# Kernel tuning notes

Hardware: AMD Instinct MI355X
Metric: run time of the kernel (lower is better)

## Reference

```python
import jax, jax.numpy as jnp
import numpy as np
from jax import lax

GEN_POLY = ("1111001", "1011011")  # rate 1/2, constraint length 7 (octal 171/133)


def build_trellis(gen_poly):
    """Feed-forward (non-recursive) convolutional trellis tables.

    State = shift-register contents, most-recent bit is the MSB of the state
    index. Returns int32 tables, each [ns, ni]:
      to_nodes[s, b]        : next state from state s with input bit b
      op_by_fromnode[s, b]  : emitted output-symbol index for (s, b)
      from_nodes[j, m]      : m-th predecessor state of state j
      ip_by_tonode[j, m]    : input bit taken on that predecessor transition
    """
    mu = len(gen_poly[0]) - 1
    ns, ni = 2 ** mu, 2
    g = np.array([[int(c) for c in p] for p in gen_poly])  # [conv_n, mu+1]
    to_nodes = np.zeros((ns, ni), np.int32)
    op_by_fromnode = np.zeros((ns, ni), np.int32)
    from_nodes = np.zeros((ns, ni), np.int32)
    ip_by_tonode = np.zeros((ns, ni), np.int32)
    fill = np.zeros(ns, np.int32)
    for s in range(ns):
        rbits = [(s >> (mu - 1 - j)) & 1 for j in range(mu)]
        for b in range(ni):
            w = np.array([b] + rbits)                 # full window [b, r0..r_{mu-1}]
            obits = (g @ w) % 2                        # output bits, MSB first
            o = int("".join(str(int(x)) for x in obits), 2)
            j = int("".join(str(x) for x in ([b] + rbits[:-1])), 2)
            to_nodes[s, b] = j
            op_by_fromnode[s, b] = o
            from_nodes[j, fill[j]] = s
            ip_by_tonode[j, fill[j]] = b
            fill[j] += 1
    return to_nodes, op_by_fromnode, from_nodes, ip_by_tonode


TO_NODES, OP_BY_FROM, FROM_NODES, IP_BY_TO = build_trellis(GEN_POLY)
CONV_N = len(GEN_POLY)
MU = len(GEN_POLY[0]) - 1
NS = 2 ** MU
NO = 2 ** CONV_N
# output-symbol bit patterns, MSB first, mapped to signs (1-2*bit)
_OP_BITS = np.array([[(o >> (CONV_N - 1 - j)) & 1 for j in range(CONV_N)]
                     for o in range(NO)], np.float32)
OP_SIGN = jnp.asarray(1.0 - 2.0 * _OP_BITS)  # [NO, CONV_N]
IP_SIGN = jnp.asarray([1.0, -1.0])           # sign of input bit b: 1-2b


def setup_inputs() -> dict:
    key = jax.random.key(0)
    k1, k2 = jax.random.split(key)
    B, n = 256, 4096
    T = n // CONV_N  # = k = 2048 info bits
    llr_ch = jax.random.normal(k1, (B, n), dtype=jnp.float32)
    llr_a = jax.random.normal(k2, (B, T), dtype=jnp.float32)
    return {"llr_ch": llr_ch, "llr_a": llr_a}


def _bcjr(llr_ch, llr_a):
    B, n = llr_ch.shape
    T = n // CONV_N
    # branch metrics: bm[t, b, o] = exp(0.5 * sum_j llr[b, t, j] * (1-2*opbit_j(o)))
    llr_r = llr_ch.reshape(B, T, CONV_N)
    bm = jnp.exp(0.5 * jnp.einsum('btj,oj->tbo', llr_r, OP_SIGN))  # [T, B, NO]
    llr_a_t = llr_a.T  # [T, B]

    def gamma_fn(bm_t, la_t):
        # a-priori factor exp(0.5*llr_a*(1-2b)) times channel branch metric
        ap = jnp.exp(0.5 * la_t[:, None, None] * IP_SIGN[None, None, :])  # [B,1,2]
        return ap * bm_t[:, OP_BY_FROM]  # [B, NS, 2]

    alpha0 = jnp.zeros((B, NS), jnp.float32).at[:, 0].set(1.0)

    def fwd(alpha_prev, inp):
        bm_t, la_t = inp
        gam = gamma_fn(bm_t, la_t)                        # [B, NS, 2] by from-state
        ag = gam * alpha_prev[:, :, None]                  # alpha_{t} * gamma_t
        agt = ag[:, FROM_NODES, IP_BY_TO]                  # regroup by to-state
        alpha = agt.sum(-1)
        alpha = alpha / alpha.sum(-1, keepdims=True)       # normalize (as in TF code)
        return alpha, alpha_prev                            # emit alpha BEFORE step t

    _, alphas = lax.scan(fwd, alpha0, (bm, llr_a_t))       # alphas[t] = alpha_t, [T,B,NS]

    beta_T = jnp.full((B, NS), 1.0 / NS, jnp.float32)      # non-terminated: uniform

    def bwd(beta_next, inp):
        bm_t, la_t, alpha_t = inp
        gam = gamma_fn(bm_t, la_t)                         # [B, NS, 2]
        bg = gam * beta_next[:, TO_NODES]                  # gamma * beta_{t+1}(to)
        beta = bg.sum(-1)
        beta = beta / beta.sum(-1, keepdims=True)
        joint = alpha_t[:, :, None] * bg                   # APP per (state, bit)
        llr_t = jnp.log(joint[..., 0].sum(-1)) - jnp.log(joint[..., 1].sum(-1))
        return beta, llr_t

    _, llrs_rev = lax.scan(bwd, beta_T, (bm[::-1], llr_a_t[::-1], alphas[::-1]))
    return llrs_rev[::-1].T  # [B, T] soft LLRs (hard_out=False)


def reference(llr_ch, llr_a):
    return _bcjr(llr_ch, llr_a)
```

## Files before the change

### kernel.cpp

```cpp
#include <hip/hip_runtime.h>
#include <hip/hip_bf16.h>

#define T_LEN 2048
#define NSTATE 64
#define NCHUNK 16
#define CH_S 128
#define WARM 64
#define RK 16

__device__ __forceinline__ float wave_sum64(float v) {
    #pragma unroll
    for (int d = 1; d < 64; d <<= 1) v += __shfl_xor(v, d, 64);
    return v;
}

__device__ __forceinline__ float pair_sum_xor1(float v) {
    int r = __builtin_amdgcn_update_dpp(0, __float_as_int(v), 0xB1, 0xF, 0xF, true);
    return v + __int_as_float(r);
}

__device__ __forceinline__ unsigned short bf16_of(float f) {
    return (unsigned short)((__float_as_uint(f) + 0x8000u) >> 16);
}
__device__ __forceinline__ float bf16_lo(unsigned u) { return __uint_as_float(u << 16); }
__device__ __forceinline__ float bf16_hi(unsigned u) { return __uint_as_float(u & 0xffff0000u); }


__global__ __launch_bounds__(256, 8)
void bcjr_sweep_kernel(const float* __restrict__ llr_ch,
                       const float* __restrict__ llr_a,
                       unsigned short* __restrict__ wsA,
                       unsigned short* __restrict__ wsB)
{
    const int wave  = blockIdx.x * 4 + (threadIdx.x >> 6);
    const int lane  = threadIdx.x & 63;
    const int dir   = wave & 1;
    const int chunk = (wave >> 1) & (NCHUNK - 1);
    const int b     = wave >> 5;

    const float c0 = 1.0f - 2.0f * (float)(__popc(lane & 57) & 1);
    const float c1 = 1.0f - 2.0f * (float)(__popc(lane & 27) & 1);
    const float kE = 0.5f * 1.442695040888963f;
    const float k0 = kE * c0, k1 = kE * c1;

    const float* chp = llr_ch + (size_t)b * (2 * T_LEN);
    const float* lap = llr_a  + (size_t)b * T_LEN;

    if (dir == 0) {
        unsigned short* w = wsA + (size_t)b * T_LEN * NSTATE;
        const int  fs0 = 2 * (lane & 31);
        const bool fhi = (lane >= 32);
        const int t0 = chunk * CH_S;
        const int ts = (chunk == 0) ? t0 : t0 - WARM;
        float state = (chunk == 0) ? ((lane == 0) ? 1.0f : 0.0f) : (1.0f / 64.0f);

        for (int g = ts; g < t0 + CH_S; g += RK) {
            const bool store = (g >= t0);
            #pragma unroll
            for (int h = 0; h < 2; ++h) {
                const int gb = g + 8 * h;
                const float4* c4 = (const float4*)(chp + 2 * gb);
                const float4* a4 = (const float4*)(lap + gb);
                float4 cc[4], aa[2];
                #pragma unroll
                for (int i = 0; i < 4; ++i) cc[i] = c4[i];
                #pragma unroll
                for (int i = 0; i < 2; ++i) aa[i] = a4[i];
                unsigned short* wb = w + (size_t)gb * NSTATE + lane;
                #pragma unroll
                for (int i = 0; i < 8; ++i) {
                    float l0 = (i & 1) ? cc[i >> 1].z : cc[i >> 1].x;
                    float l1 = (i & 1) ? cc[i >> 1].w : cc[i >> 1].y;
                    float la = ((const float*)aa)[i];
                    if (store) wb[i * NSTATE] = bf16_of(state);
                    float x   = fmaf(la, kE, fmaf(l0, k0, l1 * k1));
                    float g0v = exp2f(x);
                    float g1v = __builtin_amdgcn_rcpf(g0v);
                    float s0  = pair_sum_xor1(state * g0v);
                    float s1  = pair_sum_xor1(state * g1v);
                    float a0  = __shfl(s0, fs0, 64);
                    float a1  = __shfl(s1, fs0, 64);
                    state = fhi ? a1 : a0;
                }
            }
            float s = wave_sum64(state);
            state = state * __builtin_amdgcn_rcpf(s);
        }
    } else {
        unsigned short* w = wsB + (size_t)b * T_LEN * NSTATE;
        const int bs0 = lane >> 1;
        const int bs1 = 32 + (lane >> 1);
        const int t0 = chunk * CH_S;
        const int te = (chunk == NCHUNK - 1) ? (t0 + CH_S) : (t0 + CH_S + WARM);
        float state = 1.0f / 64.0f;

        for (int g = te - RK; g >= t0; g -= RK) {
            const bool store = (g < t0 + CH_S);
            #pragma unroll
            for (int h = 1; h >= 0; --h) {
                const int gb = g + 8 * h;
                const float4* c4 = (const float4*)(chp + 2 * gb);
                const float4* a4 = (const float4*)(lap + gb);
                float4 cc[4], aa[2];
                #pragma unroll
                for (int i = 0; i < 4; ++i) cc[i] = c4[i];
                #pragma unroll
                for (int i = 0; i < 2; ++i) aa[i] = a4[i];
                unsigned short* wb = w + (size_t)gb * NSTATE + lane;
                #pragma unroll
                for (int i = 7; i >= 0; --i) {
                    float l0 = (i & 1) ? cc[i >> 1].z : cc[i >> 1].x;
                    float l1 = (i & 1) ? cc[i >> 1].w : cc[i >> 1].y;
                    float la = ((const float*)aa)[i];
                    if (store) wb[i * NSTATE] = bf16_of(state);
                    float x   = fmaf(la, kE, fmaf(l0, k0, l1 * k1));
                    float g0v = exp2f(x);
                    float g1v = __builtin_amdgcn_rcpf(g0v);
                    float t0v = __shfl(state, bs0, 64);
                    float t1v = __shfl(state, bs1, 64);
                    state = fmaf(g0v, t0v, g1v * t1v);
                }
            }
            float s = wave_sum64(state);
            state = state * __builtin_amdgcn_rcpf(s);
        }
    }
}

__global__ __launch_bounds__(256, 8)
void bcjr_llr_kernel(const float* __restrict__ llr_ch,
                     const float* __restrict__ llr_a,
                     const unsigned short* __restrict__ wsA,
                     const unsigned short* __restrict__ wsB,
                     float* __restrict__ out)
{
    const int gid = blockIdx.x * 256 + threadIdx.x;
    const int rt  = gid >> 3;
    const int q   = gid & 7;

    const uint4 av = ((const uint4*)(wsA + (size_t)rt * NSTATE))[q];
    const uint2 b0 = ((const uint2*)(wsB + (size_t)rt * NSTATE))[q];
    const uint2 b1 = ((const uint2*)(wsB + (size_t)rt * NSTATE + 32))[q];

    float2 c2 = ((const float2*)llr_ch)[rt];
    float  la = llr_a[rt];
    const float kE = 0.5f * 1.442695040888963f;
    float E = la * kE, X0 = c2.x * kE, X1 = c2.y * kE;

    const unsigned p0 = (unsigned)(__popc(q) & 1) << 31;
    const unsigned p1 = (unsigned)(__popc(q & 3) & 1) << 31;
    float sX0 = __uint_as_float(__float_as_uint(X0) ^ p0);
    float sX1 = __uint_as_float(__float_as_uint(X1) ^ p1);

    float Ge = exp2f(E + sX0 + sX1);
    float Go = exp2f(E + sX0 - sX1);
    float Re = __builtin_amdgcn_rcpf(Ge);
    float Ro = __builtin_amdgcn_rcpf(Go);
    float e2E = exp2f(E + E);
    float r2E = __builtin_amdgcn_rcpf(e2E);
    float GBe = e2E * Re, GBo = e2E * Ro;
    float RBe = r2E * Ge, RBo = r2E * Go;

    const unsigned aw[4]  = { av.x, av.y, av.z, av.w };
    const unsigned bw0[2] = { b0.x, b0.y };
    const unsigned bw1[2] = { b1.x, b1.y };

    float n0 = 0.0f, n1 = 0.0f;
    #pragma unroll
    for (int m = 0; m < 4; ++m) {
        float GA = (m & 1) ? Go  : Ge;
        float GB = (m & 1) ? GBo : GBe;
        float RA = (m & 1) ? Ro  : Re;
        float RB = (m & 1) ? RBo : RBe;
        float a0 = bf16_lo(aw[m]);
        float a1 = bf16_hi(aw[m]);
        unsigned bd0 = bw0[m >> 1];
        unsigned bd1 = bw1[m >> 1];
        float b0v = (m & 1) ? bf16_hi(bd0) : bf16_lo(bd0);
        float b1v = (m & 1) ? bf16_hi(bd1) : bf16_lo(bd1);
        n0 = fmaf(b0v, fmaf(a0, GA, a1 * GB), n0);
        n1 = fmaf(b1v, fmaf(a0, RA, a1 * RB), n1);
    }

    #pragma unroll
    for (int d = 1; d < 8; d <<= 1) {
        n0 += __shfl_xor(n0, d, 64);
        n1 += __shfl_xor(n1, d, 64);
    }
    if (q == 0) out[rt] = __logf(n0) - __logf(n1);
}

extern "C" void kernel_launch(void* const* d_in, const int* in_sizes, int n_in,
                              void* d_out, int out_size, void* d_ws, size_t ws_size,
                              hipStream_t stream) {
    const float* llr_ch = (const float*)d_in[0];
    const float* llr_a  = (const float*)d_in[1];
    float* out = (float*)d_out;

    int B = in_sizes[0] / (2 * T_LEN);
    const size_t traj_bytes = (size_t)B * T_LEN * NSTATE * sizeof(unsigned short);

    unsigned short* wsA = (unsigned short*)d_ws;
    unsigned short* wsB = (unsigned short*)((char*)d_ws + traj_bytes);

    int n_waves = B * NCHUNK * 2;
    hipLaunchKernelGGL(bcjr_sweep_kernel, dim3(n_waves / 4), dim3(256), 0, stream,
                       llr_ch, llr_a, wsA, wsB);

    int n_thr = B * T_LEN * 8;
    hipLaunchKernelGGL(bcjr_llr_kernel, dim3(n_thr / 256), dim3(256), 0, stream,
                       llr_ch, llr_a, wsA, wsB, out);
}
```

Measured before the change: 132.3 us.

## Fuse backward sweep with LLR computation and drop beta trajectory storage

```diff
diff --git a/kernel.cpp b/kernel.cpp
--- a/kernel.cpp
+++ b/kernel.cpp
@@ -1,5 +1,4 @@
 #include <hip/hip_runtime.h>
-#include <hip/hip_bf16.h>
 
 #define T_LEN 2048
 #define NSTATE 64
@@ -8,9 +7,19 @@
 #define WARM 64
 #define RK 16
 
+template<int CTRL>
+__device__ __forceinline__ float dpp_add(float v) {
+    int r = __builtin_amdgcn_update_dpp(0, __float_as_int(v), CTRL, 0xF, 0xF, true);
+    return v + __int_as_float(r);
+}
+
 __device__ __forceinline__ float wave_sum64(float v) {
-    #pragma unroll
-    for (int d = 1; d < 64; d <<= 1) v += __shfl_xor(v, d, 64);
+    v = dpp_add<0xB1>(v);
+    v = dpp_add<0x4E>(v);
+    v = dpp_add<0x124>(v);
+    v = dpp_add<0x128>(v);
+    v += __shfl_xor(v, 16, 64);
+    v += __shfl_xor(v, 32, 64);
     return v;
 }
 
@@ -22,21 +31,17 @@
 __device__ __forceinline__ unsigned short bf16_of(float f) {
     return (unsigned short)((__float_as_uint(f) + 0x8000u) >> 16);
 }
-__device__ __forceinline__ float bf16_lo(unsigned u) { return __uint_as_float(u << 16); }
-__device__ __forceinline__ float bf16_hi(unsigned u) { return __uint_as_float(u & 0xffff0000u); }
 
 
-__global__ __launch_bounds__(256, 8)
-void bcjr_sweep_kernel(const float* __restrict__ llr_ch,
-                       const float* __restrict__ llr_a,
-                       unsigned short* __restrict__ wsA,
-                       unsigned short* __restrict__ wsB)
+__global__ __launch_bounds__(256, 4)
+void bcjr_fwd_kernel(const float* __restrict__ llr_ch,
+                     const float* __restrict__ llr_a,
+                     unsigned short* __restrict__ wsA)
 {
     const int wave  = blockIdx.x * 4 + (threadIdx.x >> 6);
     const int lane  = threadIdx.x & 63;
-    const int dir   = wave & 1;
-    const int chunk = (wave >> 1) & (NCHUNK - 1);
-    const int b     = wave >> 5;
+    const int chunk = wave & (NCHUNK - 1);
+    const int b     = wave >> 4;
 
     const float c0 = 1.0f - 2.0f * (float)(__popc(lane & 57) & 1);
     const float c1 = 1.0f - 2.0f * (float)(__popc(lane & 27) & 1);
@@ -45,149 +50,128 @@
 
     const float* chp = llr_ch + (size_t)b * (2 * T_LEN);
     const float* lap = llr_a  + (size_t)b * T_LEN;
+    unsigned short* w = wsA + (size_t)b * T_LEN * NSTATE;
 
-    if (dir == 0) {
-        unsigned short* w = wsA + (size_t)b * T_LEN * NSTATE;
-        const int  fs0 = 2 * (lane & 31);
-        const bool fhi = (lane >= 32);
-        const int t0 = chunk * CH_S;
-        const int ts = (chunk == 0) ? t0 : t0 - WARM;
-        float state = (chunk == 0) ? ((lane == 0) ? 1.0f : 0.0f) : (1.0f / 64.0f);
+    const int  fs0 = 2 * (lane & 31);
+    const bool fhi = (lane >= 32);
+    const int t0 = chunk * CH_S;
+    const int ts = (chunk == 0) ? t0 : t0 - WARM;
+    float state = (chunk == 0) ? ((lane == 0) ? 1.0f : 0.0f) : (1.0f / 64.0f);
 
-        for (int g = ts; g < t0 + CH_S; g += RK) {
-            const bool store = (g >= t0);
+    for (int g = ts; g < t0 + CH_S; g += RK) {
+        const bool store = (g >= t0);
+        #pragma unroll
+        for (int h = 0; h < 2; ++h) {
+            const int gb = g + 8 * h;
+            const float4* c4 = (const float4*)(chp + 2 * gb);
+            const float4* a4 = (const float4*)(lap + gb);
+            float4 cc[4], aa[2];
             #pragma unroll
-            for (int h = 0; h < 2; ++h) {
-                const int gb = g + 8 * h;
-                const float4* c4 = (const float4*)(chp + 2 * gb);
-                const float4* a4 = (const float4*)(lap + gb);
-                float4 cc[4], aa[2];
-                #pragma unroll
-                for (int i = 0; i < 4; ++i) cc[i] = c4[i];
-                #pragma unroll
-                for (int i = 0; i < 2; ++i) aa[i] = a4[i];
-                unsigned short* wb = w + (size_t)gb * NSTATE + lane;
-                #pragma unroll
-                for (int i = 0; i < 8; ++i) {
-                    float l0 = (i & 1) ? cc[i >> 1].z : cc[i >> 1].x;
-                    float l1 = (i & 1) ? cc[i >> 1].w : cc[i >> 1].y;
-                    float la = ((const float*)aa)[i];
-                    if (store) wb[i * NSTATE] = bf16_of(state);
-                    float x   = fmaf(la, kE, fmaf(l0, k0, l1 * k1));
-                    float g0v = exp2f(x);
-                    float g1v = __builtin_amdgcn_rcpf(g0v);
-                    float s0  = pair_sum_xor1(state * g0v);
-                    float s1  = pair_sum_xor1(state * g1v);
-                    float a0  = __shfl(s0, fs0, 64);
-                    float a1  = __shfl(s1, fs0, 64);
-                    state = fhi ? a1 : a0;
-                }
+            for (int i = 0; i < 4; ++i) cc[i] = c4[i];
+            #pragma unroll
+            for (int i = 0; i < 2; ++i) aa[i] = a4[i];
+            unsigned short* wb = w + (size_t)gb * NSTATE + lane;
+            #pragma unroll
+            for (int i = 0; i < 8; ++i) {
+                float l0 = (i & 1) ? cc[i >> 1].z : cc[i >> 1].x;
+                float l1 = (i & 1) ? cc[i >> 1].w : cc[i >> 1].y;
+                float la = ((const float*)aa)[i];
+                if (store) wb[i * NSTATE] = bf16_of(state);
+                float x   = fmaf(la, kE, fmaf(l0, k0, l1 * k1));
+                float g0v = exp2f(x);
+                float g1v = __builtin_amdgcn_rcpf(g0v);
+                float s0  = pair_sum_xor1(state * g0v);
+                float s1  = pair_sum_xor1(state * g1v);
+                float a0  = __shfl(s0, fs0, 64);
+                float a1  = __shfl(s1, fs0, 64);
+                state = fhi ? a1 : a0;
             }
-            float s = wave_sum64(state);
-            state = state * __builtin_amdgcn_rcpf(s);
         }
-    } else {
-        unsigned short* w = wsB + (size_t)b * T_LEN * NSTATE;
-        const int bs0 = lane >> 1;
-        const int bs1 = 32 + (lane >> 1);
-        const int t0 = chunk * CH_S;
-        const int te = (chunk == NCHUNK - 1) ? (t0 + CH_S) : (t0 + CH_S + WARM);
-        float state = 1.0f / 64.0f;
-
-        for (int g = te - RK; g >= t0; g -= RK) {
-            const bool store = (g < t0 + CH_S);
-            #pragma unroll
-            for (int h = 1; h >= 0; --h) {
-                const int gb = g + 8 * h;
-                const float4* c4 = (const float4*)(chp + 2 * gb);
-                const float4* a4 = (const float4*)(lap + gb);
-                float4 cc[4], aa[2];
-                #pragma unroll
-                for (int i = 0; i < 4; ++i) cc[i] = c4[i];
-                #pragma unroll
-                for (int i = 0; i < 2; ++i) aa[i] = a4[i];
-                unsigned short* wb = w + (size_t)gb * NSTATE + lane;
-                #pragma unroll
-                for (int i = 7; i >= 0; --i) {
-                    float l0 = (i & 1) ? cc[i >> 1].z : cc[i >> 1].x;
-                    float l1 = (i & 1) ? cc[i >> 1].w : cc[i >> 1].y;
-                    float la = ((const float*)aa)[i];
-                    if (store) wb[i * NSTATE] = bf16_of(state);
-                    float x   = fmaf(la, kE, fmaf(l0, k0, l1 * k1));
-                    float g0v = exp2f(x);
-                    float g1v = __builtin_amdgcn_rcpf(g0v);
-                    float t0v = __shfl(state, bs0, 64);
-                    float t1v = __shfl(state, bs1, 64);
-                    state = fmaf(g0v, t0v, g1v * t1v);
-                }
-            }
-            float s = wave_sum64(state);
-            state = state * __builtin_amdgcn_rcpf(s);
-        }
+        float s = wave_sum64(state);
+        state = state * __builtin_amdgcn_rcpf(s);
     }
 }
 
-__global__ __launch_bounds__(256, 8)
-void bcjr_llr_kernel(const float* __restrict__ llr_ch,
-                     const float* __restrict__ llr_a,
-                     const unsigned short* __restrict__ wsA,
-                     const unsigned short* __restrict__ wsB,
-                     float* __restrict__ out)
+__global__ __launch_bounds__(256, 4)
+void bcjr_bwd_llr_kernel(const float* __restrict__ llr_ch,
+                         const float* __restrict__ llr_a,
+                         const unsigned short* __restrict__ wsA,
+                         float* __restrict__ out)
 {
-    const int gid = blockIdx.x * 256 + threadIdx.x;
-    const int rt  = gid >> 3;
-    const int q   = gid & 7;
+    const int wave  = blockIdx.x * 4 + (threadIdx.x >> 6);
+    const int lane  = threadIdx.x & 63;
+    const int chunk = wave & (NCHUNK - 1);
+    const int b     = wave >> 4;
 
-    const uint4 av = ((const uint4*)(wsA + (size_t)rt * NSTATE))[q];
-    const uint2 b0 = ((const uint2*)(wsB + (size_t)rt * NSTATE))[q];
-    const uint2 b1 = ((const uint2*)(wsB + (size_t)rt * NSTATE + 32))[q];
+    const float c0 = 1.0f - 2.0f * (float)(__popc(lane & 57) & 1);
+    const float c1 = 1.0f - 2.0f * (float)(__popc(lane & 27) & 1);
+    const float kE = 0.5f * 1.442695040888963f;
+    const float k0 = kE * c0, k1 = kE * c1;
 
-    float2 c2 = ((const float2*)llr_ch)[rt];
-    float  la = llr_a[rt];
-    const float kE = 0.5f * 1.442695040888963f;
-    float E = la * kE, X0 = c2.x * kE, X1 = c2.y * kE;
+    const float* chp = llr_ch + (size_t)b * (2 * T_LEN);
+    const float* lap = llr_a  + (size_t)b * T_LEN;
+    const unsigned short* wa = wsA + (size_t)b * T_LEN * NSTATE;
+    float* outp = out + (size_t)b * T_LEN;
 
-    const unsigned p0 = (unsigned)(__popc(q) & 1) << 31;
-    const unsigned p1 = (unsigned)(__popc(q & 3) & 1) << 31;
-    float sX0 = __uint_as_float(__float_as_uint(X0) ^ p0);
-    float sX1 = __uint_as_float(__float_as_uint(X1) ^ p1);
+    const int  bs0 = lane >> 1;
+    const int  bs1 = 32 + (lane >> 1);
+    const bool fhi = (lane >= 32);
+    const int t0 = chunk * CH_S;
+    const int te = (chunk == NCHUNK - 1) ? (t0 + CH_S) : (t0 + CH_S + WARM);
+    float state = 1.0f / 64.0f;
 
-    float Ge = exp2f(E + sX0 + sX1);
-    float Go = exp2f(E + sX0 - sX1);
-    float Re = __builtin_amdgcn_rcpf(Ge);
-    float Ro = __builtin_amdgcn_rcpf(Go);
-    float e2E = exp2f(E + E);
-    float r2E = __builtin_amdgcn_rcpf(e2E);
-    float GBe = e2E * Re, GBo = e2E * Ro;
-    float RBe = r2E * Ge, RBo = r2E * Go;
-
-    const unsigned aw[4]  = { av.x, av.y, av.z, av.w };
-    const unsigned bw0[2] = { b0.x, b0.y };
-    const unsigned bw1[2] = { b1.x, b1.y };
-
-    float n0 = 0.0f, n1 = 0.0f;
-    #pragma unroll
-    for (int m = 0; m < 4; ++m) {
-        float GA = (m & 1) ? Go  : Ge;
-        float GB = (m & 1) ? GBo : GBe;
-        float RA = (m & 1) ? Ro  : Re;
-        float RB = (m & 1) ? RBo : RBe;
-        float a0 = bf16_lo(aw[m]);
-        float a1 = bf16_hi(aw[m]);
-        unsigned bd0 = bw0[m >> 1];
-        unsigned bd1 = bw1[m >> 1];
-        float b0v = (m & 1) ? bf16_hi(bd0) : bf16_lo(bd0);
-        float b1v = (m & 1) ? bf16_hi(bd1) : bf16_lo(bd1);
-        n0 = fmaf(b0v, fmaf(a0, GA, a1 * GB), n0);
-        n1 = fmaf(b1v, fmaf(a0, RA, a1 * RB), n1);
+    for (int g = te - RK; g >= t0; g -= RK) {
+        const bool act = (g < t0 + CH_S);
+        #pragma unroll
+        for (int h = 1; h >= 0; --h) {
+            const int gb = g + 8 * h;
+            const float4* c4 = (const float4*)(chp + 2 * gb);
+            const float4* a4 = (const float4*)(lap + gb);
+            float4 cc[4], aa[2];
+            #pragma unroll
+            for (int i = 0; i < 4; ++i) cc[i] = c4[i];
+            #pragma unroll
+            for (int i = 0; i < 2; ++i) aa[i] = a4[i];
+            float av[8];
+            if (act) {
+                const unsigned short* ap = wa + (size_t)gb * NSTATE + lane;
+                #pragma unroll
+                for (int i = 0; i < 8; ++i)
+                    av[i] = __uint_as_float(((unsigned)ap[i * NSTATE]) << 16);
+            }
+            #pragma unroll
+            for (int i = 7; i >= 0; --i) {
+                float l0 = (i & 1) ? cc[i >> 1].z : cc[i >> 1].x;
+                float l1 = (i & 1) ? cc[i >> 1].w : cc[i >> 1].y;
+                float la = ((const float*)aa)[i];
+                float x   = fmaf(la, kE, fmaf(l0, k0, l1 * k1));
+                float g0v = exp2f(x);
+                float g1v = __builtin_amdgcn_rcpf(g0v);
+                float t0v = __shfl(state, bs0, 64);
+                float t1v = __shfl(state, bs1, 64);
+                float p0 = g0v * t0v;
+                float p1 = g1v * t1v;
+                if (act) {
+                    float na = av[i] * p0;
+                    float nb = av[i] * p1;
+                    na += __shfl_xor(na, 32, 64);
+                    nb += __shfl_xor(nb, 32, 64);
+                    float z = fhi ? nb : na;
+                    z = dpp_add<0xB1>(z);
+                    z = dpp_add<0x4E>(z);
+                    z = dpp_add<0x124>(z);
+                    z = dpp_add<0x128>(z);
+                    z += __shfl_xor(z, 16, 64);
+                    float lg = __log2f(z);
+                    float d  = (lg - __shfl_xor(lg, 32, 64)) * 0.6931471805599453f;
+                    if (lane == 0) outp[gb + i] = d;
+                }
+                state = p0 + p1;
+            }
+        }
+        float s = wave_sum64(state);
+        state = state * __builtin_amdgcn_rcpf(s);
     }
-
-    #pragma unroll
-    for (int d = 1; d < 8; d <<= 1) {
-        n0 += __shfl_xor(n0, d, 64);
-        n1 += __shfl_xor(n1, d, 64);
-    }
-    if (q == 0) out[rt] = __logf(n0) - __logf(n1);
 }
 
 extern "C" void kernel_launch(void* const* d_in, const int* in_sizes, int n_in,
@@ -198,16 +182,11 @@
     float* out = (float*)d_out;
 
     int B = in_sizes[0] / (2 * T_LEN);
-    const size_t traj_bytes = (size_t)B * T_LEN * NSTATE * sizeof(unsigned short);
+    unsigned short* wsA = (unsigned short*)d_ws;
 
-    unsigned short* wsA = (unsigned short*)d_ws;
-    unsigned short* wsB = (unsigned short*)((char*)d_ws + traj_bytes);
-
-    int n_waves = B * NCHUNK * 2;
-    hipLaunchKernelGGL(bcjr_sweep_kernel, dim3(n_waves / 4), dim3(256), 0, stream,
-                       llr_ch, llr_a, wsA, wsB);
-
-    int n_thr = B * T_LEN * 8;
-    hipLaunchKernelGGL(bcjr_llr_kernel, dim3(n_thr / 256), dim3(256), 0, stream,
-                       llr_ch, llr_a, wsA, wsB, out);
+    int n_waves = B * NCHUNK;
+    hipLaunchKernelGGL(bcjr_fwd_kernel, dim3(n_waves / 4), dim3(256), 0, stream,
+                       llr_ch, llr_a, wsA);
+    hipLaunchKernelGGL(bcjr_bwd_llr_kernel, dim3(n_waves / 4), dim3(256), 0, stream,
+                       llr_ch, llr_a, wsA, out);
 }
```

New measurement: 147.5 us. 1.11x slower.
